# Performance work log

Measured on AMD Instinct MI355X. Metric: run time of the kernel, lower is better.

The kernel has to match this reference:

```python
import jax, jax.numpy as jnp
import numpy as np

N = 8192
D = 10
T_END = 100


def setup_inputs() -> dict:
    key = jax.random.key(0)
    k_t, k_e, k_mu, k_a, k_b = jax.random.split(key, 5)
    # sorted event times in [0, T)
    time_points = jnp.sort(jax.random.uniform(k_t, (N,), dtype=jnp.float32) * T_END)
    event_types = jax.random.randint(k_e, (N,), 0, D)
    mu = jax.random.normal(k_mu, (D,), dtype=jnp.float32)
    log_alpha = jax.random.normal(k_a, (D, D), dtype=jnp.float32)
    log_beta = jax.random.normal(k_b, (D, D), dtype=jnp.float32)
    return {
        "time_points": time_points,
        "event_types": event_types,
        "mu": mu,
        "log_alpha": log_alpha,
        "log_beta": log_beta,
        "T": T_END,
    }


def reference(time_points, event_types, mu, log_alpha, log_beta, T):
    # transform_params: softplus on raw parameters
    mu_s = jax.nn.softplus(mu)          # (D,)
    alpha = jax.nn.softplus(log_alpha)  # (D, D) receiver x trigger
    beta = jax.nn.softplus(log_beta)    # (D, D)

    n = time_points.shape[0]
    # pairwise causal time differences: dt[i, j] = t_i - t_j
    dt = time_points[:, None] - time_points[None, :]          # (N, N)
    a_mat = alpha[event_types[:, None], event_types[None, :]]  # (N, N)
    b_mat = beta[event_types[:, None], event_types[None, :]]   # (N, N)

    # strict lower-triangular causal mask (j < i)
    mask = jnp.tril(jnp.ones((n, n), dtype=bool), k=-1)
    dt_safe = jnp.where(mask, dt, 0.0)  # avoid exp overflow on masked entries
    interaction = jnp.where(mask, a_mat * b_mat * jnp.exp(-b_mat * dt_safe), 0.0)

    intensities = mu_s[event_types] + jnp.sum(interaction, axis=1)  # (N,)
    positive_ll = jnp.sum(jnp.log(intensities))

    # analytic integral of the intensity over [0, T]
    T_f = jnp.float32(T)
    delta_t = (T_f - time_points)[:, None]          # (N, 1)
    rel_alpha = alpha[:, event_types].T             # (N, D)
    rel_beta = beta[:, event_types].T               # (N, D)
    contributions = rel_alpha * (1.0 - jnp.exp(-rel_beta * delta_t))  # (N, D)
    integral = mu_s * T_f + jnp.sum(contributions, axis=0)            # (D,)

    return positive_ll - jnp.sum(integral)
```

## Files before the change

### kernel.cpp

```cpp
#include <hip/hip_runtime.h>


#define N_EV 8192
#define DT 10
#define LOG2E 1.4426950408889634f
#define R4 129

__device__ __forceinline__ float fast_exp2(float x) {
#if __has_builtin(__builtin_amdgcn_exp2f)
    return __builtin_amdgcn_exp2f(x);
#else
    return exp2f(x);
#endif
}

__device__ __forceinline__ float softplus(float x) {
    return fmaxf(x, 0.0f) + log1pf(expf(-fabsf(x)));
}

__device__ __forceinline__ float read_T(const void* p) {
    float f = *(const float*)p;
    if (f > 0.5f && f < 1.0e9f) return f;
    return (float)(*(const int*)p);
}

__global__ __launch_bounds__(256) void hawkes_pairs(
        const float* __restrict__ tp, const int* __restrict__ et,
        const float* __restrict__ la, const float* __restrict__ lb,
        float* __restrict__ partial, float* __restrict__ out) {
    const int ib = blockIdx.y, jb = blockIdx.x;
    if (jb > ib) return;

    __shared__ float  nbl2_s[DT * DT];
    __shared__ float  lab_s[DT * DT];
    __shared__ float4 tile4[DT * R4];

    const int tid = threadIdx.x;
    if (tid < DT * DT) {
        float a = softplus(la[tid]);
        float b = softplus(lb[tid]);
        nbl2_s[tid] = -b * LOG2E;
        lab_s[tid]  = log2f(a * b);
    }
    __syncthreads();

    const int j0 = jb << 8;
    {
        const float tj = tp[j0 + tid];
        const int   ej = et[j0 + tid];
        float2* tile2 = (float2*)tile4;
#pragma unroll
        for (int r = 0; r < DT; ++r) {
            float P = nbl2_s[r * DT + ej];
            float L = fmaf(-P, tj, lab_s[r * DT + ej]);
            tile2[r * (2 * R4) + tid] = make_float2(P, L);
        }
    }
    __syncthreads();

    const int i = (ib << 8) + tid;
    const float ti = tp[i];
    const float4* __restrict__ row4 = &tile4[et[i] * R4];

    const int n = (ib == jb) ? tid : 256;

    float a0 = 0.0f, a1 = 0.0f, a2 = 0.0f, a3 = 0.0f;
    const int it = n >> 2;
    for (int k = 0; k < it; ++k) {
        float4 c0 = row4[2 * k];
        float4 c1 = row4[2 * k + 1];
        a0 += fast_exp2(fmaf(c0.x, ti, c0.y));
        a1 += fast_exp2(fmaf(c0.z, ti, c0.w));
        a2 += fast_exp2(fmaf(c1.x, ti, c1.y));
        a3 += fast_exp2(fmaf(c1.z, ti, c1.w));
    }
    const float2* row2 = (const float2*)row4;
    for (int j = it << 2; j < n; ++j) {
        float2 c = row2[j];
        a0 += fast_exp2(fmaf(c.x, ti, c.y));
    }
    partial[(jb << 13) + i] = (a0 + a1) + (a2 + a3);

    if (ib == 0 && jb == 0 && tid == 0) out[0] = 0.0f;
}

__global__ __launch_bounds__(256) void hawkes_finish(
        const float* __restrict__ tp, const int* __restrict__ et,
        const float* __restrict__ mu, const float* __restrict__ la,
        const float* __restrict__ lb, const void* __restrict__ Tp,
        const float* __restrict__ partial, float* __restrict__ out) {
    __shared__ float mu_s[DT];
    __shared__ float alpha_s[DT * DT];
    __shared__ float nbl2_s[DT * DT];

    const int tid = threadIdx.x;
    if (tid < DT * DT) {
        alpha_s[tid] = softplus(la[tid]);
        nbl2_s[tid]  = -softplus(lb[tid]) * LOG2E;
    }
    if (tid >= 128 && tid < 128 + DT) mu_s[tid - 128] = softplus(mu[tid - 128]);
    __syncthreads();

    const int b = blockIdx.x;
    const int i = (b << 8) + tid;
    const float Tf = read_T(Tp);

    float acc = 0.0f;
    for (int jb = 0; jb <= b; ++jb) acc += partial[(jb << 13) + i];

    const int e = et[i];
    float val = logf(mu_s[e] + acc);

    const float delta = Tf - tp[i];
#pragma unroll
    for (int d = 0; d < DT; ++d)
        val -= alpha_s[d * DT + e] * (1.0f - fast_exp2(nbl2_s[d * DT + e] * delta));

    if (i == 0) {
        float s = 0.0f;
#pragma unroll
        for (int d = 0; d < DT; ++d) s += mu_s[d];
        val -= s * Tf;
    }

    for (int o = 32; o > 0; o >>= 1) val += __shfl_down(val, o);
    __shared__ float wsum[4];
    const int lane = tid & 63, wv = tid >> 6;
    if (lane == 0) wsum[wv] = val;
    __syncthreads();
    if (tid == 0) atomicAdd(out, wsum[0] + wsum[1] + wsum[2] + wsum[3]);
}

extern "C" void kernel_launch(void* const* d_in, const int* in_sizes, int n_in,
                              void* d_out, int out_size, void* d_ws, size_t ws_size,
                              hipStream_t stream) {
    const float* tp = (const float*)d_in[0];
    const int*   et = (const int*)d_in[1];
    const float* mu = (const float*)d_in[2];
    const float* la = (const float*)d_in[3];
    const float* lb = (const float*)d_in[4];
    const void*  Tp = d_in[5];
    float* out = (float*)d_out;
    float* ws  = (float*)d_ws;

    dim3 grid(32, 32);
    hawkes_pairs<<<grid, 256, 0, stream>>>(tp, et, la, lb, ws, out);
    hawkes_finish<<<32, 256, 0, stream>>>(tp, et, mu, la, lb, Tp, ws, out);
}
```

Measured before the change: 81.70 us.

## Replace O(N^2) off-diagonal pair sums with per-tile exponential summary statistics

```diff
diff --git a/kernel.cpp b/kernel.cpp
--- a/kernel.cpp
+++ b/kernel.cpp
@@ -24,30 +24,71 @@
     return (float)(*(const int*)p);
 }
 
-__global__ __launch_bounds__(256) void hawkes_pairs(
+__global__ __launch_bounds__(256) void hawkes_tilestats(
         const float* __restrict__ tp, const int* __restrict__ et,
-        const float* __restrict__ la, const float* __restrict__ lb,
-        float* __restrict__ partial, float* __restrict__ out) {
-    const int ib = blockIdx.y, jb = blockIdx.x;
-    if (jb > ib) return;
+        const float* __restrict__ lb,
+        float* __restrict__ S_tile, float* __restrict__ out) {
+    __shared__ float nbl2_s[DT * DT];
+    __shared__ float S_lds[DT * DT];
+    const int k = blockIdx.x, tid = threadIdx.x;
 
-    __shared__ float  nbl2_s[DT * DT];
-    __shared__ float  lab_s[DT * DT];
-    __shared__ float4 tile4[DT * R4];
-
-    const int tid = threadIdx.x;
     if (tid < DT * DT) {
-        float a = softplus(la[tid]);
-        float b = softplus(lb[tid]);
-        nbl2_s[tid] = -b * LOG2E;
-        lab_s[tid]  = log2f(a * b);
+        nbl2_s[tid] = -softplus(lb[tid]) * LOG2E;
+        S_lds[tid] = 0.0f;
     }
     __syncthreads();
 
-    const int j0 = jb << 8;
+    const int j = (k << 8) + tid;
+    const float dtr = tp[(k << 8) + 255] - tp[j];
+    const int ej = et[j];
+#pragma unroll
+    for (int r = 0; r < DT; ++r)
+        atomicAdd(&S_lds[r * DT + ej], fast_exp2(nbl2_s[r * DT + ej] * dtr));
+    __syncthreads();
+
+    if (tid < DT * DT) S_tile[k * (DT * DT) + tid] = S_lds[tid];
+    if (k == 0 && tid == 0) out[0] = 0.0f;
+}
+
+__global__ __launch_bounds__(256) void hawkes_finish(
+        const float* __restrict__ tp, const int* __restrict__ et,
+        const float* __restrict__ mu, const float* __restrict__ la,
+        const float* __restrict__ lb, const void* __restrict__ Tp,
+        const float* __restrict__ S_tile, float* __restrict__ out) {
+    __shared__ float  nbl2_s[DT * DT];
+    __shared__ float  lab_s[DT * DT];
+    __shared__ float  alpha_s[DT * DT];
+    __shared__ float  cs[DT * DT];
+    __shared__ float  mu_s[DT];
+    __shared__ float  tref_s[32];
+    __shared__ float4 tile4[DT * R4];
+
+    const int ib = blockIdx.x, tid = threadIdx.x;
+
+    float a = 0.0f, b = 0.0f;
+    if (tid < DT * DT) {
+        a = softplus(la[tid]);
+        b = softplus(lb[tid]);
+        nbl2_s[tid]  = -b * LOG2E;
+        lab_s[tid]   = log2f(a * b);
+        alpha_s[tid] = a;
+    }
+    if (tid < 32) tref_s[tid] = tp[(tid << 8) + 255];
+    if (tid >= 128 && tid < 128 + DT) mu_s[tid - 128] = softplus(mu[tid - 128]);
+    __syncthreads();
+
+    if (tid < DT * DT) {
+        const float P = nbl2_s[tid];
+        const float trefp = tref_s[ib > 0 ? ib - 1 : 0];
+        float s = 0.0f;
+        for (int k = 0; k < ib; ++k)
+            s += fast_exp2(P * (trefp - tref_s[k])) * S_tile[k * (DT * DT) + tid];
+        cs[tid] = a * b * s;
+    }
+
     {
-        const float tj = tp[j0 + tid];
-        const int   ej = et[j0 + tid];
+        const float tj = tp[(ib << 8) + tid];
+        const int   ej = et[(ib << 8) + tid];
         float2* tile2 = (float2*)tile4;
 #pragma unroll
         for (int r = 0; r < DT; ++r) {
@@ -60,15 +101,16 @@
 
     const int i = (ib << 8) + tid;
     const float ti = tp[i];
-    const float4* __restrict__ row4 = &tile4[et[i] * R4];
+    const int e = et[i];
+    const float Tf = read_T(Tp);
 
-    const int n = (ib == jb) ? tid : 256;
-
+    const float4* __restrict__ row4 = &tile4[e * R4];
+    const int n = tid;
     float a0 = 0.0f, a1 = 0.0f, a2 = 0.0f, a3 = 0.0f;
     const int it = n >> 2;
-    for (int k = 0; k < it; ++k) {
-        float4 c0 = row4[2 * k];
-        float4 c1 = row4[2 * k + 1];
+    for (int kk = 0; kk < it; ++kk) {
+        float4 c0 = row4[2 * kk];
+        float4 c1 = row4[2 * kk + 1];
         a0 += fast_exp2(fmaf(c0.x, ti, c0.y));
         a1 += fast_exp2(fmaf(c0.z, ti, c0.w));
         a2 += fast_exp2(fmaf(c1.x, ti, c1.y));
@@ -79,39 +121,18 @@
         float2 c = row2[j];
         a0 += fast_exp2(fmaf(c.x, ti, c.y));
     }
-    partial[(jb << 13) + i] = (a0 + a1) + (a2 + a3);
+    float acc = (a0 + a1) + (a2 + a3);
 
-    if (ib == 0 && jb == 0 && tid == 0) out[0] = 0.0f;
-}
+    if (ib > 0) {
+        const float dtp = ti - tref_s[ib - 1];
+#pragma unroll
+        for (int d = 0; d < DT; ++d)
+            acc += cs[e * DT + d] * fast_exp2(nbl2_s[e * DT + d] * dtp);
+    }
 
-__global__ __launch_bounds__(256) void hawkes_finish(
-        const float* __restrict__ tp, const int* __restrict__ et,
-        const float* __restrict__ mu, const float* __restrict__ la,
-        const float* __restrict__ lb, const void* __restrict__ Tp,
-        const float* __restrict__ partial, float* __restrict__ out) {
-    __shared__ float mu_s[DT];
-    __shared__ float alpha_s[DT * DT];
-    __shared__ float nbl2_s[DT * DT];
-
-    const int tid = threadIdx.x;
-    if (tid < DT * DT) {
-        alpha_s[tid] = softplus(la[tid]);
-        nbl2_s[tid]  = -softplus(lb[tid]) * LOG2E;
-    }
-    if (tid >= 128 && tid < 128 + DT) mu_s[tid - 128] = softplus(mu[tid - 128]);
-    __syncthreads();
-
-    const int b = blockIdx.x;
-    const int i = (b << 8) + tid;
-    const float Tf = read_T(Tp);
-
-    float acc = 0.0f;
-    for (int jb = 0; jb <= b; ++jb) acc += partial[(jb << 13) + i];
-
-    const int e = et[i];
     float val = logf(mu_s[e] + acc);
 
-    const float delta = Tf - tp[i];
+    const float delta = Tf - ti;
 #pragma unroll
     for (int d = 0; d < DT; ++d)
         val -= alpha_s[d * DT + e] * (1.0f - fast_exp2(nbl2_s[d * DT + e] * delta));
@@ -143,7 +164,6 @@
     float* out = (float*)d_out;
     float* ws  = (float*)d_ws;
 
-    dim3 grid(32, 32);
-    hawkes_pairs<<<grid, 256, 0, stream>>>(tp, et, la, lb, ws, out);
+    hawkes_tilestats<<<32, 256, 0, stream>>>(tp, et, lb, ws, out);
     hawkes_finish<<<32, 256, 0, stream>>>(tp, et, mu, la, lb, Tp, ws, out);
 }
```

New measurement: 75.90 us. 1.08x faster.
